# Kernel tuning notes

Hardware: AMD Instinct MI355X
Metric: run time of the kernel (lower is better)

## Reference

```python
import jax, jax.numpy as jnp
import numpy as np

L, B, N, D, H = 2, 4, 2048, 1024, 16
DH = D // H
HID = 4 * D
EPS = 1e-5


def setup_inputs() -> dict:
    key = jax.random.key(0)
    ks = jax.random.split(key, 8)
    s = 0.02
    return {
        "tokens": jax.random.normal(ks[0], (B, N, D), jnp.float32),
        "ln1_g": jnp.ones((L, D), jnp.float32),
        "ln1_b": jnp.zeros((L, D), jnp.float32),
        "qkv_w": jax.random.normal(ks[1], (L, 3 * D, D), jnp.float32) * s,
        "qkv_b": jnp.zeros((L, 3 * D), jnp.float32),
        "out_w": jax.random.normal(ks[2], (L, D, D), jnp.float32) * s,
        "out_b": jnp.zeros((L, D), jnp.float32),
        "ln2_g": jnp.ones((L, D), jnp.float32),
        "ln2_b": jnp.zeros((L, D), jnp.float32),
        "fc1_w": jax.random.normal(ks[3], (L, HID, D), jnp.float32) * s,
        "fc1_b": jnp.zeros((L, HID), jnp.float32),
        "fc2_w": jax.random.normal(ks[4], (L, D, HID), jnp.float32) * s,
        "fc2_b": jnp.zeros((L, D), jnp.float32),
    }


def _layernorm(x, g, b):
    mu = jnp.mean(x, axis=-1, keepdims=True)
    var = jnp.mean(jnp.square(x - mu), axis=-1, keepdims=True)
    return (x - mu) * jax.lax.rsqrt(var + EPS) * g + b


def _mha(x, qkv_w, qkv_b, out_w, out_b):
    # nn.MultiheadAttention self-attention, batch_first=True
    qkv = x @ qkv_w.T + qkv_b                        # [B,N,3D]
    q, k, v = jnp.split(qkv, 3, axis=-1)
    q = q.reshape(B, N, H, DH)
    k = k.reshape(B, N, H, DH)
    v = v.reshape(B, N, H, DH)
    scores = jnp.einsum("bqhd,bkhd->bhqk", q, k) / np.sqrt(DH).astype(np.float32)
    attn = jax.nn.softmax(scores, axis=-1)
    o = jnp.einsum("bhqk,bkhd->bqhd", attn, v).reshape(B, N, D)
    return o @ out_w.T + out_b


def reference(tokens, ln1_g, ln1_b, qkv_w, qkv_b, out_w, out_b,
              ln2_g, ln2_b, fc1_w, fc1_b, fc2_w, fc2_b):
    x = tokens
    for i in range(L):
        # NOTE: the original reassigns tokens = norm1(tokens) before residual,
        # so the residual is taken on the NORMED tokens (faithful to source).
        x = _layernorm(x, ln1_g[i], ln1_b[i])
        x = x + _mha(x, qkv_w[i], qkv_b[i], out_w[i], out_b[i])
        x = _layernorm(x, ln2_g[i], ln2_b[i])
        h = jax.nn.gelu(x @ fc1_w[i].T + fc1_b[i], approximate=False)
        x = x + (h @ fc2_w[i].T + fc2_b[i])
    return x  # proj_out / norm_out are Identity since out_dim == dim
```

## Files before the change

### kernel.cpp

```cpp
#include <hip/hip_runtime.h>
#include <cstdint>
#include <cstddef>

typedef unsigned short u16;
typedef __attribute__((ext_vector_type(8))) short bf16x8;
typedef __attribute__((ext_vector_type(8))) u16  u16x8;
typedef __attribute__((ext_vector_type(4))) u16  u16x4;
typedef __attribute__((ext_vector_type(4))) float f32x4;
typedef __attribute__((ext_vector_type(16))) float f32x16;
typedef __attribute__((ext_vector_type(4))) unsigned u32x4;

static __device__ __forceinline__ u16 f2bf(float f) {
  unsigned u = __builtin_bit_cast(unsigned, f);
  u += 0x7fffu + ((u >> 16) & 1u);
  return (u16)(u >> 16);
}
static __device__ __forceinline__ float bf2f(u16 h) {
  return __builtin_bit_cast(float, (unsigned)h << 16);
}
static __device__ __forceinline__ unsigned cvtpk_bf16(float a, float b) {
  unsigned r;
  asm("v_cvt_pk_bf16_f32 %0, %1, %2" : "=v"(r) : "v"(a), "v"(b));
  return r;
}
static __device__ __forceinline__ float rawexp2(float x) {
  float r;
  asm("v_exp_f32 %0, %1" : "=v"(r) : "v"(x));
  return r;
}

static __device__ __forceinline__ void gload16(u16* lds, const u16* g) {
  __builtin_amdgcn_global_load_lds(
      (__attribute__((address_space(1))) unsigned int*)(void*)(g),
      (__attribute__((address_space(3))) unsigned int*)(lds), 16, 0, 0);
}

__global__ __launch_bounds__(256) void cast_f32_bf16(
    const float* __restrict__ s, u16* __restrict__ d, int n4) {
  int i = blockIdx.x * 256 + threadIdx.x;
  if (i < n4) {
    float4 v = ((const float4*)s)[i];
    u16x4 o;
    o[0] = f2bf(v.x); o[1] = f2bf(v.y); o[2] = f2bf(v.z); o[3] = f2bf(v.w);
    ((u16x4*)d)[i] = o;
  }
}

__global__ __launch_bounds__(256) void ln_kernel(
    const float* __restrict__ in, const float* __restrict__ g,
    const float* __restrict__ bb, float* __restrict__ outf,
    u16* __restrict__ outb) {
  const int row = blockIdx.x;
  const int t = threadIdx.x;
  const float4 v = ((const float4*)(in + (size_t)row * 1024))[t];
  float s  = v.x + v.y + v.z + v.w;
  float sq = v.x * v.x + v.y * v.y + v.z * v.z + v.w * v.w;
#pragma unroll
  for (int off = 32; off > 0; off >>= 1) {
    s  += __shfl_down(s, off);
    sq += __shfl_down(sq, off);
  }
  __shared__ float red[8];
  const int w = t >> 6;
  if ((t & 63) == 0) { red[w] = s; red[4 + w] = sq; }
  __syncthreads();
  const float ts  = red[0] + red[1] + red[2] + red[3];
  const float tsq = red[4] + red[5] + red[6] + red[7];
  const float mu = ts * (1.0f / 1024.0f);
  const float rv = rsqrtf(tsq * (1.0f / 1024.0f) - mu * mu + 1e-5f);
  const float4 gv = ((const float4*)g)[t];
  const float4 bv = ((const float4*)bb)[t];
  float4 y;
  y.x = (v.x - mu) * rv * gv.x + bv.x;
  y.y = (v.y - mu) * rv * gv.y + bv.y;
  y.z = (v.z - mu) * rv * gv.z + bv.z;
  y.w = (v.w - mu) * rv * gv.w + bv.w;
  ((float4*)(outf + (size_t)row * 1024))[t] = y;
  u16x4 ob;
  ob[0] = f2bf(y.x); ob[1] = f2bf(y.y); ob[2] = f2bf(y.z); ob[3] = f2bf(y.w);
  *(u16x4*)(outb + (size_t)row * 1024 + t * 4) = ob;
}

#define BM 128
#define BN 128
#define BK 64

template <int MODE>
__global__ __launch_bounds__(256) void gemm_bt(
    const u16* __restrict__ A, const u16* __restrict__ W,
    const float* __restrict__ bias, const float* __restrict__ res,
    u16* __restrict__ outb, float* __restrict__ outf, int Nn, int K) {
  __shared__ u16 As[2 * BM * BK];
  __shared__ u16 Bs[2 * BN * BK];
  const int t  = threadIdx.x;
  const int w  = t >> 6;
  const int ln = t & 63;
  const int lr = ln & 15;
  const int lg = ln >> 4;
  const int lin  = (int)blockIdx.x;
  const int slot = lin >> 3;
  const int bm   = (((lin & 7) << 3) | (slot & 7)) * BM;
  const int bn   = (slot >> 3) * BN;
  const int wm = (w >> 1) * 64;
  const int wn = (w & 1) * 64;

  f32x4 acc[4][4] = {};

  const int srow = t >> 3;
  const int scol = 8 * ((t & 7) ^ (srow & 7));
  const u16* gA = A + (size_t)(bm + srow) * K + scol;
  const u16* gB = W + (size_t)(bn + srow) * K + scol;

  auto stage = [&](int kt) {
    u16* dA = As + (kt & 1) * 8192;
    u16* dB = Bs + (kt & 1) * 8192;
    const u16* ga = gA + kt * BK;
    const u16* gb = gB + kt * BK;
#pragma unroll
    for (int c = 0; c < 4; ++c) {
      gload16(dA + c * 2048 + w * 512, ga + (size_t)(c * 32) * K);
      gload16(dB + c * 2048 + w * 512, gb + (size_t)(c * 32) * K);
    }
  };

  const int kSteps = K >> 6;
  stage(0);
  __syncthreads();

  for (int kt = 0; kt < kSteps; ++kt) {
    if (kt + 1 < kSteps) stage(kt + 1);
    const char* AsB = (const char*)(As + (kt & 1) * 8192);
    const char* BsB = (const char*)(Bs + (kt & 1) * 8192);

#pragma unroll
    for (int kc = 0; kc < 2; ++kc) {
      bf16x8 af[4], bfr[4];
#pragma unroll
      for (int mi = 0; mi < 4; ++mi) {
        const int row = wm + mi * 16 + lr;
        af[mi] = *(const bf16x8*)(
            AsB + ((row * 128 + kc * 64 + lg * 16) ^ ((row & 7) << 4)));
      }
#pragma unroll
      for (int ni = 0; ni < 4; ++ni) {
        const int row = wn + ni * 16 + lr;
        bfr[ni] = *(const bf16x8*)(
            BsB + ((row * 128 + kc * 64 + lg * 16) ^ ((row & 7) << 4)));
      }
#pragma unroll
      for (int mi = 0; mi < 4; ++mi)
#pragma unroll
        for (int ni = 0; ni < 4; ++ni)
          acc[mi][ni] = __builtin_amdgcn_mfma_f32_16x16x32_bf16(
              af[mi], bfr[ni], acc[mi][ni], 0, 0, 0);
    }
    __syncthreads();
  }

#pragma unroll
  for (int ni = 0; ni < 4; ++ni) {
    const int col = bn + wn + ni * 16 + lr;
    const float bv = bias[col];
#pragma unroll
    for (int mi = 0; mi < 4; ++mi) {
      const int row0 = bm + wm + mi * 16 + lg * 4;
#pragma unroll
      for (int r = 0; r < 4; ++r) {
        float v = acc[mi][ni][r] + bv;
        const size_t idx = (size_t)(row0 + r) * Nn + col;
        if (MODE == 1) v = 0.5f * v * (1.0f + erff(v * 0.70710678118654752f));
        if (MODE == 2) outf[idx] = res[idx] + v;
        else           outb[idx] = f2bf(v);
      }
    }
  }
}

__global__ __launch_bounds__(256)
__attribute__((amdgpu_waves_per_eu(4, 4))) void attn_kernel(
    const u16* __restrict__ qkv, u16* __restrict__ o) {
  __shared__ u16 Ks[2 * 64 * 64];
  __shared__ u16 Vt[2 * 64 * 64];
  const int t   = threadIdx.x;
  const int w   = t >> 6;
  const int l   = t & 63;
  const int q31 = l & 31;
  const int h   = l >> 5;
  const int Lid = blockIdx.x;
  const int v_id = (Lid & 7) * 128 + (Lid >> 3);
  const int bh = v_id >> 4;
  const int b  = bh >> 4;
  const int hd = bh & 15;
  const int qb = (v_id & 15) * 128;
  const size_t baseRow = (size_t)b * 2048;
  const int hcol = hd * 64;
  const float FIXMAX = 16.0f;

  bf16x8 qf[4];
  {
    const u16* qp = qkv + (baseRow + qb + w * 32 + q31) * 3072 + hcol + h * 8;
    const float qscale = 0.125f * 1.44269504088896f;
#pragma unroll
    for (int f = 0; f < 4; ++f) {
      u16x8 raw = *(const u16x8*)(qp + f * 16);
      bf16x8 q;
#pragma unroll
      for (int i = 0; i < 8; ++i)
        q[i] = (short)f2bf(bf2f(raw[i]) * qscale);
      qf[f] = q;
    }
  }

  f32x16 oacc[2] = {};
  float lrun = 0.0f;

  const int skey = t >> 3;
  const int dK   = 8 * ((t & 7) ^ (skey & 7));
  const int sd0  = (t & 7) * 8;

  {
    gload16(Ks + w * 512,        qkv + (baseRow + skey) * 3072      + 1024 + hcol + dK);
    gload16(Ks + 2048 + w * 512, qkv + (baseRow + 32 + skey) * 3072 + 1024 + hcol + dK);
    u16x8 va = *(const u16x8*)(qkv + (baseRow + skey) * 3072      + 2048 + hcol + sd0);
    u16x8 vb = *(const u16x8*)(qkv + (baseRow + 32 + skey) * 3072 + 2048 + hcol + sd0);
    char* VtB = (char*)Vt;
#pragma unroll
    for (int j = 0; j < 8; ++j) {
      const int sw = (j ^ (t & 7)) << 4;
      *(u16*)(VtB + ((((sd0 + j) * 128 + skey * 2)        ) ^ sw)) = va[j];
      *(u16*)(VtB + ((((sd0 + j) * 128 + (32 + skey) * 2) ) ^ sw)) = vb[j];
    }
  }
  __syncthreads();

  for (int kt = 0; kt < 32; ++kt) {
    char* const KsB = (char*)Ks + (kt & 1) * 8192;
    char* const VtB = (char*)Vt + (kt & 1) * 8192;
    u16* const KsN  = Ks + ((kt & 1) ^ 1) * 4096;
    char* const VtN = (char*)Vt + ((kt & 1) ^ 1) * 8192;

    u16x8 vva, vvb;
    const bool pf = (kt < 31);
    if (pf) {
      const size_t krow = baseRow + (size_t)(kt + 1) * 64;
      gload16(KsN + w * 512,        qkv + (krow + skey) * 3072      + 1024 + hcol + dK);
      gload16(KsN + 2048 + w * 512, qkv + (krow + 32 + skey) * 3072 + 1024 + hcol + dK);
      vva = *(const u16x8*)(qkv + (krow + skey) * 3072      + 2048 + hcol + sd0);
      vvb = *(const u16x8*)(qkv + (krow + 32 + skey) * 3072 + 2048 + hcol + sd0);
    }

    f32x16 s0 = {}, s1 = {};
#pragma unroll
    for (int f = 0; f < 4; ++f) {
      const int d0b = (f * 16 + h * 8) * 2;
      {
        const int row = q31;
        bf16x8 ka = *(const bf16x8*)(KsB + ((row * 128 + d0b) ^ ((row & 7) << 4)));
        s0 = __builtin_amdgcn_mfma_f32_32x32x16_bf16(ka, qf[f], s0, 0, 0, 0);
      }
      {
        const int row = 32 + q31;
        bf16x8 ka = *(const bf16x8*)(KsB + ((row * 128 + d0b) ^ ((row & 7) << 4)));
        s1 = __builtin_amdgcn_mfma_f32_32x32x16_bf16(ka, qf[f], s1, 0, 0, 0);
      }
    }

#pragma unroll
    for (int r = 0; r < 16; ++r) {
      s0[r] = rawexp2(s0[r] - FIXMAX);
      s1[r] = rawexp2(s1[r] - FIXMAX);
    }
    float tsum[16];
#pragma unroll
    for (int r = 0; r < 16; ++r) tsum[r] = s0[r] + s1[r];
#pragma unroll
    for (int st = 8; st >= 1; st >>= 1)
#pragma unroll
      for (int r = 0; r < st; ++r) tsum[r] += tsum[r + st];
    lrun += tsum[0] + __shfl_xor(tsum[0], 32);

#pragma unroll
    for (int kw = 0; kw < 4; ++kw) {
      const int w1 = kw & 1;
      const f32x16 sv = (kw < 2) ? s0 : s1;
      const unsigned L0 = cvtpk_bf16(sv[8 * w1 + 0], sv[8 * w1 + 1]);
      const unsigned L1 = cvtpk_bf16(sv[8 * w1 + 2], sv[8 * w1 + 3]);
      const unsigned H0 = cvtpk_bf16(sv[8 * w1 + 4], sv[8 * w1 + 5]);
      const unsigned H1 = cvtpk_bf16(sv[8 * w1 + 6], sv[8 * w1 + 7]);
      const unsigned X0 = h ? L0 : H0;
      const unsigned X1 = h ? L1 : H1;
      const unsigned R0 = (unsigned)__shfl_xor((int)X0, 32);
      const unsigned R1 = (unsigned)__shfl_xor((int)X1, 32);
      u32x4 pw;
      pw[0] = h ? R0 : L0;
      pw[1] = h ? R1 : L1;
      pw[2] = h ? H0 : R0;
      pw[3] = h ? H1 : R1;
      const bf16x8 pb = __builtin_bit_cast(bf16x8, pw);
      const int k0b = (kw * 16 + h * 8) * 2;
#pragma unroll
      for (int dt = 0; dt < 2; ++dt) {
        const int d = dt * 32 + q31;
        bf16x8 va = *(const bf16x8*)(
            VtB + ((d * 128 + k0b) ^ ((((d & 7) ^ ((d >> 3) & 7))) << 4)));
        oacc[dt] = __builtin_amdgcn_mfma_f32_32x32x16_bf16(va, pb, oacc[dt], 0, 0, 0);
      }
    }

    if (pf) {
#pragma unroll
      for (int j = 0; j < 8; ++j) {
        const int sw = (j ^ (t & 7)) << 4;
        *(u16*)(VtN + ((((sd0 + j) * 128 + skey * 2)        ) ^ sw)) = vva[j];
        *(u16*)(VtN + ((((sd0 + j) * 128 + (32 + skey) * 2) ) ^ sw)) = vvb[j];
      }
    }
    __syncthreads();
  }

  const float inv = 1.0f / lrun;
  const size_t orow = baseRow + qb + w * 32 + q31;
#pragma unroll
  for (int dt = 0; dt < 2; ++dt)
#pragma unroll
    for (int g = 0; g < 4; ++g) {
      u16x4 ov;
#pragma unroll
      for (int j = 0; j < 4; ++j) ov[j] = f2bf(oacc[dt][g * 4 + j] * inv);
      *(u16x4*)(o + orow * 1024 + hcol + dt * 32 + g * 8 + h * 4) = ov;
    }
}

extern "C" void kernel_launch(void* const* d_in, const int* in_sizes, int n_in,
                              void* d_out, int out_size, void* d_ws,
                              size_t ws_size, hipStream_t stream) {
  const float* tokens = (const float*)d_in[0];
  const float* ln1_g  = (const float*)d_in[1];
  const float* ln1_b  = (const float*)d_in[2];
  const float* qkv_w  = (const float*)d_in[3];
  const float* qkv_b  = (const float*)d_in[4];
  const float* out_w  = (const float*)d_in[5];
  const float* out_b  = (const float*)d_in[6];
  const float* ln2_g  = (const float*)d_in[7];
  const float* ln2_b  = (const float*)d_in[8];
  const float* fc1_w  = (const float*)d_in[9];
  const float* fc1_b  = (const float*)d_in[10];
  const float* fc2_w  = (const float*)d_in[11];
  const float* fc2_b  = (const float*)d_in[12];
  float* xf = (float*)d_out;

  char* ws = (char*)d_ws;
  size_t off = 0;
  auto take = [&](size_t bytes) {
    char* p = ws + off;
    off += (bytes + 255) & ~(size_t)255;
    return p;
  };
  u16* xn    = (u16*)take((size_t)8192 * 1024 * 2);
  u16* big   = (u16*)take((size_t)8192 * 4096 * 2);
  u16* attnb = (u16*)take((size_t)8192 * 1024 * 2);
  u16* qkvw  = (u16*)take((size_t)2 * 3072 * 1024 * 2);
  u16* outw  = (u16*)take((size_t)2 * 1024 * 1024 * 2);
  u16* fc1w  = (u16*)take((size_t)2 * 4096 * 1024 * 2);
  u16* fc2w  = (u16*)take((size_t)2 * 1024 * 4096 * 2);
  u16* qkvb16 = big;
  u16* hb     = big;

  cast_f32_bf16<<<6144, 256, 0, stream>>>(qkv_w, qkvw, 2 * 3072 * 1024 / 4);
  cast_f32_bf16<<<2048, 256, 0, stream>>>(out_w, outw, 2 * 1024 * 1024 / 4);
  cast_f32_bf16<<<8192, 256, 0, stream>>>(fc1_w, fc1w, 2 * 4096 * 1024 / 4);
  cast_f32_bf16<<<8192, 256, 0, stream>>>(fc2_w, fc2w, 2 * 1024 * 4096 / 4);

  for (int i = 0; i < 2; ++i) {
    ln_kernel<<<8192, 256, 0, stream>>>(i == 0 ? tokens : xf,
                                        ln1_g + i * 1024, ln1_b + i * 1024, xf, xn);
    gemm_bt<0><<<1536, 256, 0, stream>>>(
        xn, qkvw + (size_t)i * 3072 * 1024, qkv_b + i * 3072, nullptr,
        qkvb16, nullptr, 3072, 1024);
    attn_kernel<<<1024, 256, 0, stream>>>(qkvb16, attnb);
    gemm_bt<2><<<512, 256, 0, stream>>>(
        attnb, outw + (size_t)i * 1024 * 1024, out_b + i * 1024, xf,
        nullptr, xf, 1024, 1024);
    ln_kernel<<<8192, 256, 0, stream>>>(xf, ln2_g + i * 1024, ln2_b + i * 1024,
                                        xf, xn);
    gemm_bt<1><<<2048, 256, 0, stream>>>(
        xn, fc1w + (size_t)i * 4096 * 1024, fc1_b + i * 4096, nullptr,
        hb, nullptr, 4096, 1024);
    gemm_bt<2><<<512, 256, 0, stream>>>(
        hb, fc2w + (size_t)i * 1024 * 4096, fc2_b + i * 1024, xf,
        nullptr, xf, 1024, 4096);
  }
}
```

Baseline: 883.2 us.

## Switch GEMM to 4-stage BK=32 pipeline with explicit vmcnt waits

The GEMM main loop moves from a double-buffered BK=64 scheme with full __syncthreads to a four-buffer ring of BK=32 tiles that keeps three stages in flight, using s_waitcnt vmcnt and raw s_barrier instead of a full sync. The LDS swizzle and load mapping are reworked for the narrower 64-byte rows. The aim is to hide global-load latency better and avoid draining all outstanding loads each iteration. In exchange there are twice as many barriers per K, and the wait-count bookkeeping is fragile.

```diff
diff --git a/kernel.cpp b/kernel.cpp
--- a/kernel.cpp
+++ b/kernel.cpp
@@ -27,6 +27,10 @@
   float r;
   asm("v_exp_f32 %0, %1" : "=v"(r) : "v"(x));
   return r;
+}
+template <int N>
+static __device__ __forceinline__ void gwait() {
+  asm volatile("s_waitcnt vmcnt(%0)" ::"i"(N) : "memory");
 }
 
 static __device__ __forceinline__ void gload16(u16* lds, const u16* g) {
@@ -83,15 +87,15 @@
 
 #define BM 128
 #define BN 128
-#define BK 64
+#define BK 32
 
 template <int MODE>
 __global__ __launch_bounds__(256) void gemm_bt(
     const u16* __restrict__ A, const u16* __restrict__ W,
     const float* __restrict__ bias, const float* __restrict__ res,
     u16* __restrict__ outb, float* __restrict__ outf, int Nn, int K) {
-  __shared__ u16 As[2 * BM * BK];
-  __shared__ u16 Bs[2 * BN * BK];
+  __shared__ u16 As[4 * BM * BK];
+  __shared__ u16 Bs[4 * BN * BK];
   const int t  = threadIdx.x;
   const int w  = t >> 6;
   const int ln = t & 63;
@@ -106,56 +110,60 @@
 
   f32x4 acc[4][4] = {};
 
-  const int srow = t >> 3;
-  const int scol = 8 * ((t & 7) ^ (srow & 7));
+  const int srow = t >> 2;
+  const int scol = 8 * ((t & 3) ^ ((t >> 3) & 3));
   const u16* gA = A + (size_t)(bm + srow) * K + scol;
   const u16* gB = W + (size_t)(bn + srow) * K + scol;
 
   auto stage = [&](int kt) {
-    u16* dA = As + (kt & 1) * 8192;
-    u16* dB = Bs + (kt & 1) * 8192;
+    u16* dA = As + (kt & 3) * 4096;
+    u16* dB = Bs + (kt & 3) * 4096;
     const u16* ga = gA + kt * BK;
     const u16* gb = gB + kt * BK;
-#pragma unroll
-    for (int c = 0; c < 4; ++c) {
-      gload16(dA + c * 2048 + w * 512, ga + (size_t)(c * 32) * K);
-      gload16(dB + c * 2048 + w * 512, gb + (size_t)(c * 32) * K);
-    }
+    gload16(dA + w * 512,        ga);
+    gload16(dA + 2048 + w * 512, ga + (size_t)64 * K);
+    gload16(dB + w * 512,        gb);
+    gload16(dB + 2048 + w * 512, gb + (size_t)64 * K);
   };
 
-  const int kSteps = K >> 6;
-  stage(0);
-  __syncthreads();
-
-  for (int kt = 0; kt < kSteps; ++kt) {
-    if (kt + 1 < kSteps) stage(kt + 1);
-    const char* AsB = (const char*)(As + (kt & 1) * 8192);
-    const char* BsB = (const char*)(Bs + (kt & 1) * 8192);
-
-#pragma unroll
-    for (int kc = 0; kc < 2; ++kc) {
-      bf16x8 af[4], bfr[4];
-#pragma unroll
-      for (int mi = 0; mi < 4; ++mi) {
-        const int row = wm + mi * 16 + lr;
-        af[mi] = *(const bf16x8*)(
-            AsB + ((row * 128 + kc * 64 + lg * 16) ^ ((row & 7) << 4)));
-      }
-#pragma unroll
-      for (int ni = 0; ni < 4; ++ni) {
-        const int row = wn + ni * 16 + lr;
-        bfr[ni] = *(const bf16x8*)(
-            BsB + ((row * 128 + kc * 64 + lg * 16) ^ ((row & 7) << 4)));
-      }
-#pragma unroll
-      for (int mi = 0; mi < 4; ++mi)
-#pragma unroll
-        for (int ni = 0; ni < 4; ++ni)
-          acc[mi][ni] = __builtin_amdgcn_mfma_f32_16x16x32_bf16(
-              af[mi], bfr[ni], acc[mi][ni], 0, 0, 0);
-    }
-    __syncthreads();
-  }
+  auto compute = [&](int kt) {
+    const char* AsB = (const char*)As + (kt & 3) * 8192;
+    const char* BsB = (const char*)Bs + (kt & 3) * 8192;
+    bf16x8 af[4], bfr[4];
+#pragma unroll
+    for (int mi = 0; mi < 4; ++mi) {
+      const int row = wm + mi * 16 + lr;
+      af[mi] = *(const bf16x8*)(
+          AsB + ((row * 64 + lg * 16) ^ (((row >> 1) & 3) << 4)));
+    }
+#pragma unroll
+    for (int ni = 0; ni < 4; ++ni) {
+      const int row = wn + ni * 16 + lr;
+      bfr[ni] = *(const bf16x8*)(
+          BsB + ((row * 64 + lg * 16) ^ (((row >> 1) & 3) << 4)));
+    }
+#pragma unroll
+    for (int mi = 0; mi < 4; ++mi)
+#pragma unroll
+      for (int ni = 0; ni < 4; ++ni)
+        acc[mi][ni] = __builtin_amdgcn_mfma_f32_16x16x32_bf16(
+            af[mi], bfr[ni], acc[mi][ni], 0, 0, 0);
+  };
+
+  const int T = K >> 5;
+  stage(0); stage(1); stage(2);
+  gwait<8>();
+  __builtin_amdgcn_s_barrier();
+  int kt = 0;
+  for (; kt < T - 3; ++kt) {
+    stage(kt + 3);
+    compute(kt);
+    gwait<8>();
+    __builtin_amdgcn_s_barrier();
+  }
+  compute(kt);      gwait<4>(); __builtin_amdgcn_s_barrier();
+  compute(kt + 1);  gwait<0>(); __builtin_amdgcn_s_barrier();
+  compute(kt + 2);
 
 #pragma unroll
   for (int ni = 0; ni < 4; ++ni) {
```

Result: slower. 1.009 ms (+14.3%).
